# Kernel optimization log

Hardware: AMD Instinct MI355X
Metric: run time of the kernel (lower is better)

Reference implementation:

```python
import jax, jax.numpy as jnp
import numpy as np

D_IN, H1, H2, D_OUT = 1024, 4096, 512, 256
GS = H1 // H2  # group size = 8

def setup_inputs() -> dict:
    key = jax.random.key(0)
    ks = jax.random.split(key, 7)
    s1 = 1.0 / np.sqrt(D_IN)
    s2 = 1.0 / np.sqrt(GS)
    s3 = 1.0 / np.sqrt(H2)
    return {
        "x": jax.random.normal(ks[0], (16384, D_IN), dtype=jnp.float32),
        "W1": jax.random.uniform(ks[1], (H1, D_IN), minval=-s1, maxval=s1, dtype=jnp.float32),
        "b1": jax.random.uniform(ks[2], (H1,), minval=-s1, maxval=s1, dtype=jnp.float32),
        "W2": jax.random.uniform(ks[3], (H2, GS), minval=-s2, maxval=s2, dtype=jnp.float32),
        "b2": jax.random.uniform(ks[4], (H2,), minval=-s2, maxval=s2, dtype=jnp.float32),
        "W3": jax.random.uniform(ks[5], (D_OUT, H2), minval=-s3, maxval=s3, dtype=jnp.float32),
        "b3": jax.random.uniform(ks[6], (D_OUT,), minval=-s3, maxval=s3, dtype=jnp.float32),
    }

def reference(x, W1, b1, W2, b2, W3, b3):
    # fc1 + sigmoid: [B, H1]
    h = jax.nn.sigmoid(x @ W1.T + b1)
    # grouped tiny linears as one batched contraction: chunk dim=1 into H2 groups of GS
    hg = h.reshape(h.shape[0], H2, GS)            # [B, G, gs]
    x2 = jax.nn.sigmoid(jnp.einsum('bgs,gs->bg', hg, W2) + b2)  # [B, H2]
    # fc3 (no activation)
    return x2 @ W3.T + b3                          # [B, D_OUT]
```

## Files before the change

### kernel.cpp

```cpp
#include <hip/hip_runtime.h>
#include <cstdint>


#define B_ROWS 16384
#define DIN 1024
#define H1  4096
#define H2  512
#define DOUT 256
#define TILE 128
#define BK 64
#define BK1 128
#define INV_W1SCALE 0.015625f

#define NX4  (B_ROWS * DIN / 4)
#define NW14 (H1 * DIN / 4)
#define NW34 (DOUT * H2 / 4)

typedef __bf16 bf16x8 __attribute__((ext_vector_type(8)));
typedef float f32x4 __attribute__((ext_vector_type(4)));

__device__ __forceinline__ unsigned short f2bf(float f) {
    union { float f; uint32_t u; } v; v.f = f;
    uint32_t u = v.u;
    u += 0x7FFFu + ((u >> 16) & 1u);
    return (unsigned short)(u >> 16);
}

__device__ __forceinline__ float sigmoidf_fast(float x) {
    return 1.0f / (1.0f + __expf(-x));
}

__global__ __launch_bounds__(256) void cvt3_kernel(
    const float* __restrict__ x, const float* __restrict__ w1,
    const float* __restrict__ w3, unsigned int* __restrict__ xo,
    unsigned int* __restrict__ w1o, unsigned short* __restrict__ w3o) {
    int i = blockIdx.x * 256 + threadIdx.x;
    if (i < NX4) {
        float4 v = ((const float4*)x)[i];
        unsigned int p = 0;
        p = __builtin_amdgcn_cvt_pk_fp8_f32(v.x, v.y, p, false);
        p = __builtin_amdgcn_cvt_pk_fp8_f32(v.z, v.w, p, true);
        xo[i] = p;
    } else if (i < NX4 + NW14) {
        int j = i - NX4;
        float4 v = ((const float4*)w1)[j];
        unsigned int p = 0;
        p = __builtin_amdgcn_cvt_pk_fp8_f32(v.x * 64.0f, v.y * 64.0f, p, false);
        p = __builtin_amdgcn_cvt_pk_fp8_f32(v.z * 64.0f, v.w * 64.0f, p, true);
        w1o[j] = p;
    } else {
        int j = i - NX4 - NW14;
        float4 v = ((const float4*)w3)[j];
        ushort4 o;
        o.x = f2bf(v.x); o.y = f2bf(v.y); o.z = f2bf(v.z); o.w = f2bf(v.w);
        ((ushort4*)w3o)[j] = o;
    }
}

__device__ __forceinline__ void load_lds16(const void* g, void* l) {
    __builtin_amdgcn_global_load_lds(
        (const __attribute__((address_space(1))) void*)g,
        (__attribute__((address_space(3))) void*)l, 16, 0, 0);
}

__global__ __launch_bounds__(256, 2) void gemm1_fused(
    const unsigned char* __restrict__ Xq,
    const unsigned char* __restrict__ W1q,
    const float* __restrict__ b1,
    const float* __restrict__ W2,
    const float* __restrict__ b2,
    unsigned short* __restrict__ X2) {
    __shared__ __attribute__((aligned(16))) unsigned char lsA[TILE * BK1];
    __shared__ __attribute__((aligned(16))) unsigned char lsB[TILE * BK1];
    const int tid = threadIdx.x, lane = tid & 63, wave = tid >> 6;
    const int wm = (wave >> 1) * 64, wn = (wave & 1) * 64;

    const int bid = blockIdx.x;
    const int xcd = bid & 7;
    const int local = bid >> 3;
    const int n0 = (xcd * 4 + (local & 3)) * TILE;
    const int a0 = (local >> 2) * TILE;

    const int q = lane >> 4, m16 = lane & 15;

    int gA[4], gB[4], lo[4];
#pragma unroll
    for (int i = 0; i < 4; ++i) {
        const int ch = wave * 4 + i;
        const int r  = ch * 8 + (lane >> 3);
        const int kc = ((lane & 7) - (lane >> 3)) & 7;
        gA[i] = (a0 + r) * DIN + kc * 16;
        gB[i] = (n0 + r) * DIN + kc * 16;
        lo[i] = ch * 1024;
    }
    int rowA[4], rowB[4], so[4];
#pragma unroll
    for (int t = 0; t < 4; ++t) {
        rowA[t] = (wm + t * 16 + m16) * BK1 + (q & 1) * 8;
        rowB[t] = (wn + t * 16 + m16) * BK1 + (q & 1) * 8;
    }
#pragma unroll
    for (int s = 0; s < 4; ++s)
        so[s] = ((s * 2 + (q >> 1) + (m16 & 7)) & 7) * 16;

    f32x4 acc[4][4];
#pragma unroll
    for (int r = 0; r < 4; ++r)
#pragma unroll
        for (int c = 0; c < 4; ++c) acc[r][c] = (f32x4)0.0f;

    for (int kt = 0; kt < DIN / BK1; ++kt) {
        __syncthreads();
        const int k0 = kt * BK1;
#pragma unroll
        for (int i = 0; i < 4; ++i) {
            load_lds16(Xq + gA[i] + k0, lsA + lo[i]);
            load_lds16(W1q + gB[i] + k0, lsB + lo[i]);
        }
        __syncthreads();
#pragma unroll
        for (int s = 0; s < 4; ++s) {
            long af[4], bfr[4];
#pragma unroll
            for (int t = 0; t < 4; ++t) af[t]  = *(const long*)(lsA + rowA[t] + so[s]);
#pragma unroll
            for (int t = 0; t < 4; ++t) bfr[t] = *(const long*)(lsB + rowB[t] + so[s]);
#pragma unroll
            for (int r = 0; r < 4; ++r)
#pragma unroll
                for (int c = 0; c < 4; ++c)
                    acc[r][c] = __builtin_amdgcn_mfma_f32_16x16x32_fp8_fp8(
                        af[r], bfr[c], acc[r][c], 0, 0, 0);
        }
    }

#pragma unroll
    for (int c = 0; c < 4; ++c) {
        const int gn = n0 + wn + c * 16 + m16;
        const float w2v = W2[gn];
        const float b1v = b1[gn];
        const int g = gn >> 3;
        const float b2v = b2[g];
#pragma unroll
        for (int r = 0; r < 4; ++r) {
#pragma unroll
            for (int i = 0; i < 4; ++i) {
                const int gm = a0 + wm + r * 16 + q * 4 + i;
                float h = sigmoidf_fast(acc[r][c][i] * INV_W1SCALE + b1v);
                float v = h * w2v;
                v += __shfl_xor(v, 1, 64);
                v += __shfl_xor(v, 2, 64);
                v += __shfl_xor(v, 4, 64);
                if ((lane & 7) == 0)
                    X2[gm * H2 + g] = f2bf(sigmoidf_fast(v + b2v));
            }
        }
    }
}

template <int K>
__device__ __forceinline__ void gemm_core(const unsigned short* __restrict__ A,
                                          const unsigned short* __restrict__ Bm,
                                          unsigned short* lsA, unsigned short* lsB,
                                          int a_row0, int b_row0,
                                          int lane, int wave, int wm, int wn,
                                          f32x4 acc[4][4]) {
    const int q = lane >> 4, m16 = lane & 15;
    int gA[4], gB[4], lo[4];
#pragma unroll
    for (int i = 0; i < 4; ++i) {
        const int ch = wave * 4 + i;
        const int r  = ch * 8 + (lane >> 3);
        const int kc = ((lane & 7) - (lane >> 3)) & 7;
        gA[i] = (a_row0 + r) * K + kc * 8;
        gB[i] = (b_row0 + r) * K + kc * 8;
        lo[i] = ch * 512;
    }
    int ra[2][4], rb[2][4];
#pragma unroll
    for (int h = 0; h < 2; ++h)
#pragma unroll
        for (int t = 0; t < 4; ++t) {
            const int s = ((h * 4 + q + (m16 & 7)) & 7) * 8;
            ra[h][t] = (wm + t * 16 + m16) * BK + s;
            rb[h][t] = (wn + t * 16 + m16) * BK + s;
        }
    for (int kt = 0; kt < K / BK; ++kt) {
        __syncthreads();
        const int k0 = kt * BK;
#pragma unroll
        for (int i = 0; i < 4; ++i) {
            load_lds16(A + gA[i] + k0, lsA + lo[i]);
            load_lds16(Bm + gB[i] + k0, lsB + lo[i]);
        }
        __syncthreads();
#pragma unroll
        for (int h = 0; h < 2; ++h) {
            bf16x8 af[4], bfr[4];
#pragma unroll
            for (int t = 0; t < 4; ++t) af[t]  = *(const bf16x8*)(lsA + ra[h][t]);
#pragma unroll
            for (int t = 0; t < 4; ++t) bfr[t] = *(const bf16x8*)(lsB + rb[h][t]);
#pragma unroll
            for (int r = 0; r < 4; ++r)
#pragma unroll
                for (int c = 0; c < 4; ++c)
                    acc[r][c] = __builtin_amdgcn_mfma_f32_16x16x32_bf16(
                        af[r], bfr[c], acc[r][c], 0, 0, 0);
        }
    }
}

__global__ __launch_bounds__(256, 2) void gemm3_kernel(
    const unsigned short* __restrict__ X2,
    const unsigned short* __restrict__ W3b,
    const float* __restrict__ b3,
    float* __restrict__ Out) {
    __shared__ __attribute__((aligned(16))) unsigned short lsA[TILE * BK];
    __shared__ __attribute__((aligned(16))) unsigned short lsB[TILE * BK];
    const int tid = threadIdx.x, lane = tid & 63, wave = tid >> 6;
    const int wm = (wave >> 1) * 64, wn = (wave & 1) * 64;
    const int a0 = blockIdx.y * TILE;
    const int n0 = blockIdx.x * TILE;

    f32x4 acc[4][4];
#pragma unroll
    for (int r = 0; r < 4; ++r)
#pragma unroll
        for (int c = 0; c < 4; ++c) acc[r][c] = (f32x4)0.0f;

    gemm_core<H2>(X2, W3b, lsA, lsB, a0, n0, lane, wave, wm, wn, acc);

    const int q = lane >> 4, m16 = lane & 15;
#pragma unroll
    for (int c = 0; c < 4; ++c) {
        const int gn = n0 + wn + c * 16 + m16;
        const float b3v = b3[gn];
#pragma unroll
        for (int r = 0; r < 4; ++r) {
#pragma unroll
            for (int i = 0; i < 4; ++i) {
                const int gm = a0 + wm + r * 16 + q * 4 + i;
                Out[gm * DOUT + gn] = acc[r][c][i] + b3v;
            }
        }
    }
}

extern "C" void kernel_launch(void* const* d_in, const int* in_sizes, int n_in,
                              void* d_out, int out_size, void* d_ws, size_t ws_size,
                              hipStream_t stream) {
    const float* x  = (const float*)d_in[0];
    const float* W1 = (const float*)d_in[1];
    const float* b1 = (const float*)d_in[2];
    const float* W2 = (const float*)d_in[3];
    const float* b2 = (const float*)d_in[4];
    const float* W3 = (const float*)d_in[5];
    const float* b3 = (const float*)d_in[6];
    float* out = (float*)d_out;

    char* ws = (char*)d_ws;
    unsigned char*  x_q   = (unsigned char*)ws;
    unsigned char*  w1_q  = (unsigned char*)(ws + 16777216);
    unsigned short* w3_bf = (unsigned short*)(ws + 16777216 + 4194304);
    unsigned short* x2_bf = (unsigned short*)(ws + 16777216 + 4194304 + 262144);

    cvt3_kernel<<<(NX4 + NW14 + NW34) / 256, 256, 0, stream>>>(
        x, W1, W3, (unsigned int*)x_q, (unsigned int*)w1_q, w3_bf);

    gemm1_fused<<<(B_ROWS / TILE) * (H1 / TILE), 256, 0, stream>>>(
        x_q, w1_q, b1, W2, b2, x2_bf);

    gemm3_kernel<<<dim3(DOUT / TILE, B_ROWS / TILE), 256, 0, stream>>>(
        x2_bf, w3_bf, b3, out);
}
```

Measured before the change: 274.5 us.

## Double-buffer fp8 GEMM1 LDS tiles and shrink GEMM3 row tile

```diff
diff --git a/kernel.cpp b/kernel.cpp
--- a/kernel.cpp
+++ b/kernel.cpp
@@ -9,7 +9,8 @@
 #define DOUT 256
 #define TILE 128
 #define BK 64
-#define BK1 128
+#define BK1 64
+#define MT3 64
 #define INV_W1SCALE 0.015625f
 
 #define NX4  (B_ROWS * DIN / 4)
@@ -27,7 +28,7 @@
 }
 
 __device__ __forceinline__ float sigmoidf_fast(float x) {
-    return 1.0f / (1.0f + __expf(-x));
+    return __builtin_amdgcn_rcpf(1.0f + __expf(-x));
 }
 
 __global__ __launch_bounds__(256) void cvt3_kernel(
@@ -70,8 +71,8 @@
     const float* __restrict__ W2,
     const float* __restrict__ b2,
     unsigned short* __restrict__ X2) {
-    __shared__ __attribute__((aligned(16))) unsigned char lsA[TILE * BK1];
-    __shared__ __attribute__((aligned(16))) unsigned char lsB[TILE * BK1];
+    __shared__ __attribute__((aligned(16))) unsigned char lsA[2][TILE * BK1];
+    __shared__ __attribute__((aligned(16))) unsigned char lsB[2][TILE * BK1];
     const int tid = threadIdx.x, lane = tid & 63, wave = tid >> 6;
     const int wm = (wave >> 1) * 64, wn = (wave & 1) * 64;
 
@@ -83,25 +84,25 @@
 
     const int q = lane >> 4, m16 = lane & 15;
 
-    int gA[4], gB[4], lo[4];
-#pragma unroll
-    for (int i = 0; i < 4; ++i) {
-        const int ch = wave * 4 + i;
-        const int r  = ch * 8 + (lane >> 3);
-        const int kc = ((lane & 7) - (lane >> 3)) & 7;
+    int gA[2], gB[2], lo[2];
+#pragma unroll
+    for (int i = 0; i < 2; ++i) {
+        const int ch = wave * 2 + i;
+        const int r  = ch * 16 + (lane >> 2);
+        const int kc = ((lane & 3) - (lane >> 2)) & 3;
         gA[i] = (a0 + r) * DIN + kc * 16;
         gB[i] = (n0 + r) * DIN + kc * 16;
         lo[i] = ch * 1024;
     }
-    int rowA[4], rowB[4], so[4];
+    int rowA[4], rowB[4], so[2];
 #pragma unroll
     for (int t = 0; t < 4; ++t) {
-        rowA[t] = (wm + t * 16 + m16) * BK1 + (q & 1) * 8;
-        rowB[t] = (wn + t * 16 + m16) * BK1 + (q & 1) * 8;
-    }
-#pragma unroll
-    for (int s = 0; s < 4; ++s)
-        so[s] = ((s * 2 + (q >> 1) + (m16 & 7)) & 7) * 16;
+        rowA[t] = (wm + t * 16 + m16) * BK1;
+        rowB[t] = (wn + t * 16 + m16) * BK1;
+    }
+#pragma unroll
+    for (int s = 0; s < 2; ++s)
+        so[s] = ((s * 2 + (q >> 1) + (m16 & 3)) & 3) * 16 + (q & 1) * 8;
 
     f32x4 acc[4][4];
 #pragma unroll
@@ -109,22 +110,31 @@
 #pragma unroll
         for (int c = 0; c < 4; ++c) acc[r][c] = (f32x4)0.0f;
 
+#pragma unroll
+    for (int i = 0; i < 2; ++i) {
+        load_lds16(Xq + gA[i], lsA[0] + lo[i]);
+        load_lds16(W1q + gB[i], lsB[0] + lo[i]);
+    }
+
+#pragma unroll 2
     for (int kt = 0; kt < DIN / BK1; ++kt) {
+        const int p = kt & 1;
         __syncthreads();
-        const int k0 = kt * BK1;
-#pragma unroll
-        for (int i = 0; i < 4; ++i) {
-            load_lds16(Xq + gA[i] + k0, lsA + lo[i]);
-            load_lds16(W1q + gB[i] + k0, lsB + lo[i]);
-        }
-        __syncthreads();
-#pragma unroll
-        for (int s = 0; s < 4; ++s) {
+        if (kt + 1 < DIN / BK1) {
+            const int k1 = (kt + 1) * BK1;
+#pragma unroll
+            for (int i = 0; i < 2; ++i) {
+                load_lds16(Xq + gA[i] + k1, lsA[p ^ 1] + lo[i]);
+                load_lds16(W1q + gB[i] + k1, lsB[p ^ 1] + lo[i]);
+            }
+        }
+#pragma unroll
+        for (int s = 0; s < 2; ++s) {
             long af[4], bfr[4];
 #pragma unroll
-            for (int t = 0; t < 4; ++t) af[t]  = *(const long*)(lsA + rowA[t] + so[s]);
-#pragma unroll
-            for (int t = 0; t < 4; ++t) bfr[t] = *(const long*)(lsB + rowB[t] + so[s]);
+            for (int t = 0; t < 4; ++t) af[t]  = *(const long*)(lsA[p] + rowA[t] + so[s]);
+#pragma unroll
+            for (int t = 0; t < 4; ++t) bfr[t] = *(const long*)(lsB[p] + rowB[t] + so[s]);
 #pragma unroll
             for (int r = 0; r < 4; ++r)
 #pragma unroll
@@ -158,89 +168,87 @@
     }
 }
 
-template <int K>
-__device__ __forceinline__ void gemm_core(const unsigned short* __restrict__ A,
-                                          const unsigned short* __restrict__ Bm,
-                                          unsigned short* lsA, unsigned short* lsB,
-                                          int a_row0, int b_row0,
-                                          int lane, int wave, int wm, int wn,
-                                          f32x4 acc[4][4]) {
-    const int q = lane >> 4, m16 = lane & 15;
-    int gA[4], gB[4], lo[4];
-#pragma unroll
-    for (int i = 0; i < 4; ++i) {
-        const int ch = wave * 4 + i;
-        const int r  = ch * 8 + (lane >> 3);
-        const int kc = ((lane & 7) - (lane >> 3)) & 7;
-        gA[i] = (a_row0 + r) * K + kc * 8;
-        gB[i] = (b_row0 + r) * K + kc * 8;
-        lo[i] = ch * 512;
-    }
-    int ra[2][4], rb[2][4];
-#pragma unroll
-    for (int h = 0; h < 2; ++h)
-#pragma unroll
-        for (int t = 0; t < 4; ++t) {
-            const int s = ((h * 4 + q + (m16 & 7)) & 7) * 8;
-            ra[h][t] = (wm + t * 16 + m16) * BK + s;
-            rb[h][t] = (wn + t * 16 + m16) * BK + s;
-        }
-    for (int kt = 0; kt < K / BK; ++kt) {
-        __syncthreads();
-        const int k0 = kt * BK;
-#pragma unroll
-        for (int i = 0; i < 4; ++i) {
-            load_lds16(A + gA[i] + k0, lsA + lo[i]);
-            load_lds16(Bm + gB[i] + k0, lsB + lo[i]);
-        }
-        __syncthreads();
-#pragma unroll
-        for (int h = 0; h < 2; ++h) {
-            bf16x8 af[4], bfr[4];
-#pragma unroll
-            for (int t = 0; t < 4; ++t) af[t]  = *(const bf16x8*)(lsA + ra[h][t]);
-#pragma unroll
-            for (int t = 0; t < 4; ++t) bfr[t] = *(const bf16x8*)(lsB + rb[h][t]);
-#pragma unroll
-            for (int r = 0; r < 4; ++r)
-#pragma unroll
-                for (int c = 0; c < 4; ++c)
-                    acc[r][c] = __builtin_amdgcn_mfma_f32_16x16x32_bf16(
-                        af[r], bfr[c], acc[r][c], 0, 0, 0);
-        }
-    }
-}
-
 __global__ __launch_bounds__(256, 2) void gemm3_kernel(
     const unsigned short* __restrict__ X2,
     const unsigned short* __restrict__ W3b,
     const float* __restrict__ b3,
     float* __restrict__ Out) {
-    __shared__ __attribute__((aligned(16))) unsigned short lsA[TILE * BK];
+    __shared__ __attribute__((aligned(16))) unsigned short lsA[MT3 * BK];
     __shared__ __attribute__((aligned(16))) unsigned short lsB[TILE * BK];
     const int tid = threadIdx.x, lane = tid & 63, wave = tid >> 6;
-    const int wm = (wave >> 1) * 64, wn = (wave & 1) * 64;
-    const int a0 = blockIdx.y * TILE;
+    const int wn = wave * 32;
+    const int a0 = blockIdx.y * MT3;
     const int n0 = blockIdx.x * TILE;
-
-    f32x4 acc[4][4];
+    const int q = lane >> 4, m16 = lane & 15;
+
+    int gA[2], loA[2], gB[4], loB[4];
+#pragma unroll
+    for (int i = 0; i < 2; ++i) {
+        const int ch = wave * 2 + i;
+        const int r  = ch * 8 + (lane >> 3);
+        const int kc = ((lane & 7) - (lane >> 3)) & 7;
+        gA[i]  = (a0 + r) * H2 + kc * 8;
+        loA[i] = ch * 512;
+    }
+#pragma unroll
+    for (int i = 0; i < 4; ++i) {
+        const int ch = wave * 4 + i;
+        const int r  = ch * 8 + (lane >> 3);
+        const int kc = ((lane & 7) - (lane >> 3)) & 7;
+        gB[i]  = (n0 + r) * H2 + kc * 8;
+        loB[i] = ch * 512;
+    }
+    int ra[2][4], rb[2][2];
+#pragma unroll
+    for (int h = 0; h < 2; ++h) {
+        const int s = ((h * 4 + q + (m16 & 7)) & 7) * 8;
+#pragma unroll
+        for (int t = 0; t < 4; ++t) ra[h][t] = (t * 16 + m16) * BK + s;
+#pragma unroll
+        for (int c = 0; c < 2; ++c) rb[h][c] = (wn + c * 16 + m16) * BK + s;
+    }
+
+    f32x4 acc[4][2];
 #pragma unroll
     for (int r = 0; r < 4; ++r)
 #pragma unroll
-        for (int c = 0; c < 4; ++c) acc[r][c] = (f32x4)0.0f;
-
-    gemm_core<H2>(X2, W3b, lsA, lsB, a0, n0, lane, wave, wm, wn, acc);
-
-    const int q = lane >> 4, m16 = lane & 15;
-#pragma unroll
-    for (int c = 0; c < 4; ++c) {
+        for (int c = 0; c < 2; ++c) acc[r][c] = (f32x4)0.0f;
+
+    for (int kt = 0; kt < H2 / BK; ++kt) {
+        __syncthreads();
+        const int k0 = kt * BK;
+#pragma unroll
+        for (int i = 0; i < 2; ++i)
+            load_lds16(X2 + gA[i] + k0, lsA + loA[i]);
+#pragma unroll
+        for (int i = 0; i < 4; ++i)
+            load_lds16(W3b + gB[i] + k0, lsB + loB[i]);
+        __syncthreads();
+#pragma unroll
+        for (int h = 0; h < 2; ++h) {
+            bf16x8 af[4], bfr[2];
+#pragma unroll
+            for (int t = 0; t < 4; ++t) af[t]  = *(const bf16x8*)(lsA + ra[h][t]);
+#pragma unroll
+            for (int c = 0; c < 2; ++c) bfr[c] = *(const bf16x8*)(lsB + rb[h][c]);
+#pragma unroll
+            for (int r = 0; r < 4; ++r)
+#pragma unroll
+                for (int c = 0; c < 2; ++c)
+                    acc[r][c] = __builtin_amdgcn_mfma_f32_16x16x32_bf16(
+                        af[r], bfr[c], acc[r][c], 0, 0, 0);
+        }
+    }
+
+#pragma unroll
+    for (int c = 0; c < 2; ++c) {
         const int gn = n0 + wn + c * 16 + m16;
         const float b3v = b3[gn];
 #pragma unroll
         for (int r = 0; r < 4; ++r) {
 #pragma unroll
             for (int i = 0; i < 4; ++i) {
-                const int gm = a0 + wm + r * 16 + q * 4 + i;
+                const int gm = a0 + r * 16 + q * 4 + i;
                 Out[gm * DOUT + gn] = acc[r][c][i] + b3v;
             }
         }
@@ -271,6 +279,6 @@
     gemm1_fused<<<(B_ROWS / TILE) * (H1 / TILE), 256, 0, stream>>>(
         x_q, w1_q, b1, W2, b2, x2_bf);
 
-    gemm3_kernel<<<dim3(DOUT / TILE, B_ROWS / TILE), 256, 0, stream>>>(
+    gemm3_kernel<<<dim3(DOUT / TILE, B_ROWS / MT3), 256, 0, stream>>>(
         x2_bf, w3_bf, b3, out);
 }
```

Result: slower. 307.0 us (+11.8%).

## Double-buffer fp8 GEMM1 LDS tiles with pre-swizzled layout from converter

Applied to the files above, without the earlier changes.

```diff
diff --git a/kernel.cpp b/kernel.cpp
--- a/kernel.cpp
+++ b/kernel.cpp
@@ -9,15 +9,16 @@
 #define DOUT 256
 #define TILE 128
 #define BK 64
-#define BK1 128
+#define BK1 64
 #define INV_W1SCALE 0.015625f
 
-#define NX4  (B_ROWS * DIN / 4)
-#define NW14 (H1 * DIN / 4)
+#define NXP  (B_ROWS * DIN / 8)
+#define NW1P (H1 * DIN / 8)
 #define NW34 (DOUT * H2 / 4)
 
 typedef __bf16 bf16x8 __attribute__((ext_vector_type(8)));
 typedef float f32x4 __attribute__((ext_vector_type(4)));
+typedef long i64x2 __attribute__((ext_vector_type(2)));
 
 __device__ __forceinline__ unsigned short f2bf(float f) {
     union { float f; uint32_t u; } v; v.f = f;
@@ -27,29 +28,35 @@
 }
 
 __device__ __forceinline__ float sigmoidf_fast(float x) {
-    return 1.0f / (1.0f + __expf(-x));
+    return __builtin_amdgcn_rcpf(1.0f + __expf(-x));
+}
+
+__device__ __forceinline__ unsigned long long pack8_fp8(float4 v0, float4 v1, float sc) {
+    unsigned int p0 = 0, p1 = 0;
+    p0 = __builtin_amdgcn_cvt_pk_fp8_f32(v0.x * sc, v0.y * sc, p0, false);
+    p0 = __builtin_amdgcn_cvt_pk_fp8_f32(v0.z * sc, v0.w * sc, p0, true);
+    p1 = __builtin_amdgcn_cvt_pk_fp8_f32(v1.x * sc, v1.y * sc, p1, false);
+    p1 = __builtin_amdgcn_cvt_pk_fp8_f32(v1.z * sc, v1.w * sc, p1, true);
+    return (unsigned long long)p0 | ((unsigned long long)p1 << 32);
 }
 
 __global__ __launch_bounds__(256) void cvt3_kernel(
     const float* __restrict__ x, const float* __restrict__ w1,
-    const float* __restrict__ w3, unsigned int* __restrict__ xo,
-    unsigned int* __restrict__ w1o, unsigned short* __restrict__ w3o) {
+    const float* __restrict__ w3, unsigned char* __restrict__ xo,
+    unsigned char* __restrict__ w1o, unsigned short* __restrict__ w3o) {
     int i = blockIdx.x * 256 + threadIdx.x;
-    if (i < NX4) {
-        float4 v = ((const float4*)x)[i];
-        unsigned int p = 0;
-        p = __builtin_amdgcn_cvt_pk_fp8_f32(v.x, v.y, p, false);
-        p = __builtin_amdgcn_cvt_pk_fp8_f32(v.z, v.w, p, true);
-        xo[i] = p;
-    } else if (i < NX4 + NW14) {
-        int j = i - NX4;
-        float4 v = ((const float4*)w1)[j];
-        unsigned int p = 0;
-        p = __builtin_amdgcn_cvt_pk_fp8_f32(v.x * 64.0f, v.y * 64.0f, p, false);
-        p = __builtin_amdgcn_cvt_pk_fp8_f32(v.z * 64.0f, v.w * 64.0f, p, true);
-        w1o[j] = p;
+    if (i < NXP + NW1P) {
+        const float* src; unsigned char* dst; int j0; float sc;
+        if (i < NXP) { src = x;  dst = xo;  j0 = i;        sc = 1.0f; }
+        else         { src = w1; dst = w1o; j0 = i - NXP;  sc = 64.0f; }
+        const int ri = j0 >> 7, rem = j0 & 127, kb = rem >> 3, j = rem & 7;
+        const float4* s4 = (const float4*)(src + ri * DIN + kb * 64 + j * 8);
+        float4 v0 = s4[0], v1 = s4[1];
+        const int q = j & 3, s = j >> 2;
+        const int pos = ((q + (ri >> 1)) & 3) * 16 + s * 8;
+        *(unsigned long long*)(dst + ri * DIN + kb * 64 + pos) = pack8_fp8(v0, v1, sc);
     } else {
-        int j = i - NX4 - NW14;
+        int j = i - NXP - NW1P;
         float4 v = ((const float4*)w3)[j];
         ushort4 o;
         o.x = f2bf(v.x); o.y = f2bf(v.y); o.z = f2bf(v.z); o.w = f2bf(v.w);
@@ -70,8 +77,8 @@
     const float* __restrict__ W2,
     const float* __restrict__ b2,
     unsigned short* __restrict__ X2) {
-    __shared__ __attribute__((aligned(16))) unsigned char lsA[TILE * BK1];
-    __shared__ __attribute__((aligned(16))) unsigned char lsB[TILE * BK1];
+    __shared__ __attribute__((aligned(16))) unsigned char lsA[2][TILE * BK1];
+    __shared__ __attribute__((aligned(16))) unsigned char lsB[2][TILE * BK1];
     const int tid = threadIdx.x, lane = tid & 63, wave = tid >> 6;
     const int wm = (wave >> 1) * 64, wn = (wave & 1) * 64;
 
@@ -83,25 +90,23 @@
 
     const int q = lane >> 4, m16 = lane & 15;
 
-    int gA[4], gB[4], lo[4];
-#pragma unroll
-    for (int i = 0; i < 4; ++i) {
-        const int ch = wave * 4 + i;
-        const int r  = ch * 8 + (lane >> 3);
-        const int kc = ((lane & 7) - (lane >> 3)) & 7;
-        gA[i] = (a0 + r) * DIN + kc * 16;
-        gB[i] = (n0 + r) * DIN + kc * 16;
+    int gA[2], gB[2], lo[2];
+#pragma unroll
+    for (int i = 0; i < 2; ++i) {
+        const int ch = wave * 2 + i;
+        const int r  = ch * 16 + (lane >> 2);
+        gA[i] = (a0 + r) * DIN + (lane & 3) * 16;
+        gB[i] = (n0 + r) * DIN + (lane & 3) * 16;
         lo[i] = ch * 1024;
     }
-    int rowA[4], rowB[4], so[4];
+    int fa[4], fb[4];
 #pragma unroll
     for (int t = 0; t < 4; ++t) {
-        rowA[t] = (wm + t * 16 + m16) * BK1 + (q & 1) * 8;
-        rowB[t] = (wn + t * 16 + m16) * BK1 + (q & 1) * 8;
-    }
-#pragma unroll
-    for (int s = 0; s < 4; ++s)
-        so[s] = ((s * 2 + (q >> 1) + (m16 & 7)) & 7) * 16;
+        const int ra = wm + t * 16 + m16;
+        const int rb = wn + t * 16 + m16;
+        fa[t] = ra * BK1 + ((q + (ra >> 1)) & 3) * 16;
+        fb[t] = rb * BK1 + ((q + (rb >> 1)) & 3) * 16;
+    }
 
     f32x4 acc[4][4];
 #pragma unroll
@@ -109,29 +114,37 @@
 #pragma unroll
         for (int c = 0; c < 4; ++c) acc[r][c] = (f32x4)0.0f;
 
+#pragma unroll
+    for (int i = 0; i < 2; ++i) {
+        load_lds16(Xq + gA[i], lsA[0] + lo[i]);
+        load_lds16(W1q + gB[i], lsB[0] + lo[i]);
+    }
+
+#pragma unroll 2
     for (int kt = 0; kt < DIN / BK1; ++kt) {
+        const int p = kt & 1;
         __syncthreads();
-        const int k0 = kt * BK1;
-#pragma unroll
-        for (int i = 0; i < 4; ++i) {
-            load_lds16(Xq + gA[i] + k0, lsA + lo[i]);
-            load_lds16(W1q + gB[i] + k0, lsB + lo[i]);
-        }
-        __syncthreads();
-#pragma unroll
-        for (int s = 0; s < 4; ++s) {
-            long af[4], bfr[4];
-#pragma unroll
-            for (int t = 0; t < 4; ++t) af[t]  = *(const long*)(lsA + rowA[t] + so[s]);
-#pragma unroll
-            for (int t = 0; t < 4; ++t) bfr[t] = *(const long*)(lsB + rowB[t] + so[s]);
+        if (kt + 1 < DIN / BK1) {
+            const int k1 = (kt + 1) * BK1;
+#pragma unroll
+            for (int i = 0; i < 2; ++i) {
+                load_lds16(Xq + gA[i] + k1, lsA[p ^ 1] + lo[i]);
+                load_lds16(W1q + gB[i] + k1, lsB[p ^ 1] + lo[i]);
+            }
+        }
+        i64x2 va[4], vb[4];
+#pragma unroll
+        for (int t = 0; t < 4; ++t) va[t] = *(const i64x2*)(lsA[p] + fa[t]);
+#pragma unroll
+        for (int t = 0; t < 4; ++t) vb[t] = *(const i64x2*)(lsB[p] + fb[t]);
+#pragma unroll
+        for (int s = 0; s < 2; ++s)
 #pragma unroll
             for (int r = 0; r < 4; ++r)
 #pragma unroll
                 for (int c = 0; c < 4; ++c)
                     acc[r][c] = __builtin_amdgcn_mfma_f32_16x16x32_fp8_fp8(
-                        af[r], bfr[c], acc[r][c], 0, 0, 0);
-        }
+                        va[r][s], vb[c][s], acc[r][c], 0, 0, 0);
     }
 
 #pragma unroll
@@ -265,8 +278,8 @@
     unsigned short* w3_bf = (unsigned short*)(ws + 16777216 + 4194304);
     unsigned short* x2_bf = (unsigned short*)(ws + 16777216 + 4194304 + 262144);
 
-    cvt3_kernel<<<(NX4 + NW14 + NW34) / 256, 256, 0, stream>>>(
-        x, W1, W3, (unsigned int*)x_q, (unsigned int*)w1_q, w3_bf);
+    cvt3_kernel<<<(NXP + NW1P + NW34) / 256, 256, 0, stream>>>(
+        x, W1, W3, x_q, w1_q, w3_bf);
 
     gemm1_fused<<<(B_ROWS / TILE) * (H1 / TILE), 256, 0, stream>>>(
         x_q, w1_q, b1, W2, b2, x2_bf);
```

Result: slower. 282.1 us (+2.8%).
